# Performance work log

Measured on AMD Instinct MI355X. Metric: run time of the kernel, lower is better.

The kernel has to match this reference:

```python
import jax, jax.numpy as jnp
import numpy as np

TWO_PI = 2.0 * np.pi
SIGMA = 25.0  # marginal_prob_std sigma


def marginal_prob_std(t):
    # std(t) = sqrt((sigma^{2t} - 1) / (2 ln sigma)) for VE-SDE
    return jnp.sqrt((SIGMA ** (2.0 * t) - 1.0) / (2.0 * np.log(SIGMA)))


def edge_conv(x, src, dst, W1, b1, W2, b2, num_nodes):
    # PyG EdgeConv: msg = mlp(cat([x_i, x_j - x_i])), x_i = x[dst], x_j = x[src];
    # scatter-max over dst. First linear split so concat is never materialized:
    # cat([x_i, x_j - x_i]) @ W1 = x_i @ (Wa - Wb) + x_j @ Wb
    d = x.shape[-1]
    Wa, Wb = W1[:d], W1[d:]
    h_center = x @ (Wa - Wb)        # [N, H]
    h_nbr = x @ Wb                  # [N, H]
    e = jax.nn.relu(h_center[dst] + h_nbr[src] + b1)  # [E, H]
    e = e @ W2 + b2                 # [E, out]
    return jax.ops.segment_max(e, dst, num_segments=num_nodes)


def setup_inputs() -> dict:
    N, E, B, H, EM = 50000, 500000, 1024, 128, 64
    CLS, SD, GD, WD = 10, 4, 2, 2
    key = jax.random.key(0)
    ks = jax.random.split(key, 32)

    def lin(k, fi, fo):
        return jax.random.normal(k, (fi, fo), jnp.float32) / np.sqrt(fi)

    inp = {
        "t": jax.random.uniform(ks[0], (N, 1), jnp.float32, 1e-3, 1.0),
        "obj_x": jax.random.normal(ks[1], (N, SD), jnp.float32),
        "obj_geo": jax.random.normal(ks[2], (N, GD), jnp.float32),
        "wall": jax.random.normal(ks[3], (B, WD), jnp.float32),
        "category": jax.random.randint(ks[4], (N,), 0, CLS),
        "batch_idx": jnp.sort(jax.random.randint(ks[5], (N,), 0, B)),
        "src": jax.random.randint(ks[6], (E,), 0, N),
        "dst": jnp.tile(jnp.arange(N), E // N),  # every node receives edges
        "embed_W": jax.random.normal(ks[7], (CLS, EM), jnp.float32),
        "gfp_W": jax.random.normal(ks[8], (EM // 2,), jnp.float32) * 30.0,
        "sW": lin(ks[9], EM, EM), "sb": jnp.zeros((EM,), jnp.float32),
        "w1": lin(ks[10], WD, EM), "wb1": jnp.zeros((EM,), jnp.float32),
        "w2": lin(ks[11], EM, EM), "wb2": jnp.zeros((EM,), jnp.float32),
        "i1": lin(ks[12], SD + GD, H), "ib1": jnp.zeros((H,), jnp.float32),
        "i2": lin(ks[13], H, H), "ib2": jnp.zeros((H,), jnp.float32),
        "m1W1": lin(ks[14], 2 * (H + 3 * EM), H), "m1b1": jnp.zeros((H,), jnp.float32),
        "m1W2": lin(ks[15], H, H), "m1b2": jnp.zeros((H,), jnp.float32),
        "m2W1": lin(ks[16], 2 * (H + 3 * EM), H), "m2b1": jnp.zeros((H,), jnp.float32),
        "m2W2": lin(ks[17], H, SD), "m2b2": jnp.zeros((SD,), jnp.float32),
    }
    return inp


def reference(t, obj_x, obj_geo, wall, category, batch_idx, src, dst,
              embed_W, gfp_W, sW, sb, w1, wb1, w2, wb2,
              i1, ib1, i2, ib2, m1W1, m1b1, m1W2, m1b2,
              m2W1, m2b1, m2W2, m2b2):
    N = obj_x.shape[0]
    # conditioning features
    class_feat = jax.nn.relu(embed_W[category])                       # [N, EM]
    tv = t[:, 0]                                                      # [N]
    x_proj = tv[:, None] * gfp_W[None, :] * TWO_PI                    # [N, EM/2]
    gfp = jnp.concatenate([jnp.sin(x_proj), jnp.cos(x_proj)], axis=-1)
    sigma_feat = jax.nn.relu(gfp @ sW + sb)                           # [N, EM]
    wall_h = jax.nn.relu(jax.nn.relu(wall @ w1 + wb1) @ w2 + wb2)     # [B, EM]
    wall_feat = wall_h[batch_idx]                                     # [N, EM]
    cond = jnp.concatenate([class_feat, sigma_feat, wall_feat], axis=-1)

    # init encoder
    xin = jnp.concatenate([obj_x, obj_geo], axis=-1)                  # [N, 6]
    init = jax.nn.relu(jax.nn.relu(xin @ i1 + ib1) @ i2 + ib2)        # [N, H]

    # main backbone: two EdgeConvs with conditioning concat
    x = jnp.concatenate([init, cond], axis=-1)                        # [N, H+3EM]
    x = jax.nn.relu(edge_conv(x, src, dst, m1W1, m1b1, m1W2, m1b2, N))
    x = jnp.concatenate([x, cond], axis=-1)                           # [N, H+3EM]
    x = edge_conv(x, src, dst, m2W1, m2b1, m2W2, m2b2, N)             # [N, 4]

    return x / (marginal_prob_std(t) + 1e-7)
```

## Files before the change

kernel.cpp:

```cpp
#include <hip/hip_runtime.h>
#include <math.h>

#define NTHREADS 256
#define TWO_PI_F 6.28318530717958647692f
#define LOG_SIGMA 3.2188758248682006f

typedef unsigned short u16;
typedef unsigned int u32;
typedef short bf16x8 __attribute__((ext_vector_type(8)));
typedef float f32x4 __attribute__((ext_vector_type(4)));

#define MFMA(a, b, c) __builtin_amdgcn_mfma_f32_16x16x32_bf16((a), (b), (c), 0, 0, 0)

__device__ __forceinline__ u16 f2b(float f) {
  u32 u = __float_as_uint(f);
  u32 r = (u + 0x7fffu + ((u >> 16) & 1u)) >> 16;
  return (u16)r;
}
__device__ __forceinline__ float blo(u32 u) { return __uint_as_float(u << 16); }
__device__ __forceinline__ float bhi(u32 u) { return __uint_as_float(u & 0xffff0000u); }
__device__ __forceinline__ u32 pk(float lo, float hi) { return (u32)f2b(lo) | ((u32)f2b(hi) << 16); }

__global__ __launch_bounds__(256) void prep_kernel(
    const float* __restrict__ m1W2, const float* __restrict__ m1W1,
    const float* __restrict__ m2W1, const float* __restrict__ sW,
    const float* __restrict__ i1, const float* __restrict__ i2,
    u16* __restrict__ m1W2t, u16* __restrict__ Wc1t, u16* __restrict__ Wc2t,
    u16* __restrict__ sWt, u16* __restrict__ i1t, u16* __restrict__ i2t) {
  int idx = blockIdx.x * 256 + threadIdx.x;
  if (idx < 16384) {
    int n = idx >> 7, k = idx & 127;
    m1W2t[idx] = f2b(m1W2[k * 128 + n]);
  } else if (idx < 98304) {
    int j = idx - 16384;
    int n = j / 320, k = j - n * 320;
    float v = (n < 128) ? (m1W1[k * 128 + n] - m1W1[(320 + k) * 128 + n])
                        : m1W1[(320 + k) * 128 + (n - 128)];
    Wc1t[j] = f2b(v);
  } else if (idx < 180224) {
    int j = idx - 98304;
    int n = j / 320, k = j - n * 320;
    float v = (n < 128) ? (m2W1[k * 128 + n] - m2W1[(320 + k) * 128 + n])
                        : m2W1[(320 + k) * 128 + (n - 128)];
    Wc2t[j] = f2b(v);
  } else if (idx < 184320) {
    int j = idx - 180224;
    int n = j >> 6, k = j & 63;
    sWt[j] = f2b(sW[k * 64 + n]);
  } else if (idx < 188416) {
    int j = idx - 184320;
    int n = j >> 5, k = j & 31;
    i1t[j] = (k < 6) ? f2b(i1[k * 128 + n]) : (u16)0;
  } else if (idx < 204800) {
    int j = idx - 188416;
    int n = j >> 7, k = j & 127;
    i2t[j] = f2b(i2[k * 128 + n]);
  }
}

__global__ void wall_kernel(const float* __restrict__ wall,
                            const float* __restrict__ w1, const float* __restrict__ wb1,
                            const float* __restrict__ w2, const float* __restrict__ wb2,
                            float* __restrict__ wall_h) {
  __shared__ float h1[64];
  int b = blockIdx.x;
  int f = threadIdx.x;
  float v = wall[b * 2 + 0] * w1[f] + wall[b * 2 + 1] * w1[64 + f] + wb1[f];
  h1[f] = fmaxf(v, 0.f);
  __syncthreads();
  float acc = wb2[f];
  for (int k = 0; k < 64; ++k) acc = fmaf(h1[k], w2[k * 64 + f], acc);
  wall_h[b * 64 + f] = fmaxf(acc, 0.f);
}

__global__ __launch_bounds__(256) void node_kernel(
    const float* __restrict__ t, const float* __restrict__ obj_x,
    const float* __restrict__ obj_geo,
    const int* __restrict__ category, const int* __restrict__ batch_idx,
    const float* __restrict__ embed_W, const float* __restrict__ gfp_W,
    const u16* __restrict__ sWt, const float* __restrict__ sb,
    const u16* __restrict__ i1t, const float* __restrict__ ib1,
    const u16* __restrict__ i2t, const float* __restrict__ ib2,
    const u16* __restrict__ Wc1t, const float* __restrict__ m1b1,
    const float* __restrict__ wall_h,
    float* __restrict__ hc1, u16* __restrict__ hn1,
    u16* __restrict__ cond_bf, int N) {
  __shared__ u16 xb[64 * 328];
  __shared__ u16 ab[64 * 136];
  __shared__ float t_s[64];
  __shared__ int cat_s[64];
  __shared__ int bid_s[64];

  const int tid = threadIdx.x;
  const int base = blockIdx.x * 64;
  const int wave = tid >> 6, lane = tid & 63;
  const int ln16 = lane & 15, q8 = lane >> 4;

  bf16x8 bs0 = *(const bf16x8*)(sWt + (size_t)((wave * 16 + ln16) * 64) + q8 * 8);
  bf16x8 bs1 = *(const bf16x8*)(sWt + (size_t)((wave * 16 + ln16) * 64) + 32 + q8 * 8);
  bf16x8 bh[2];
#pragma unroll
  for (int nt = 0; nt < 2; ++nt)
    bh[nt] = *(const bf16x8*)(i1t + (size_t)((wave * 32 + nt * 16 + ln16) * 32) + q8 * 8);

  if (tid < 64) {
    int node = min(base + tid, N - 1);
    t_s[tid] = t[node];
    cat_s[tid] = category[node];
    bid_s[tid] = batch_idx[node];
  }
  __syncthreads();

  for (int idx = tid; idx < 64 * 32; idx += NTHREADS) {
    int row = idx >> 5, k = idx & 31;
    float xp = t_s[row] * gfp_W[k] * TWO_PI_F;
    float s, c;
    sincosf(xp, &s, &c);
    ab[row * 136 + k] = f2b(s);
    ab[row * 136 + 32 + k] = f2b(c);
  }
  for (int idx = tid; idx < 64 * 64; idx += NTHREADS) {
    int row = idx >> 6, f = idx & 63;
    xb[row * 328 + 128 + f] = f2b(fmaxf(embed_W[cat_s[row] * 64 + f], 0.f));
    xb[row * 328 + 256 + f] = f2b(wall_h[bid_s[row] * 64 + f]);
  }
  __syncthreads();

  f32x4 cs[4];
#pragma unroll
  for (int mt = 0; mt < 4; ++mt) cs[mt] = (f32x4)0.f;
#pragma unroll
  for (int mt = 0; mt < 4; ++mt) {
    bf16x8 a0 = *(const bf16x8*)&ab[(mt * 16 + ln16) * 136 + q8 * 8];
    cs[mt] = MFMA(a0, bs0, cs[mt]);
  }
#pragma unroll
  for (int mt = 0; mt < 4; ++mt) {
    bf16x8 a1 = *(const bf16x8*)&ab[(mt * 16 + ln16) * 136 + 32 + q8 * 8];
    cs[mt] = MFMA(a1, bs1, cs[mt]);
  }
  __syncthreads();

  {
    int col = wave * 16 + ln16;
    float bias = sb[col];
#pragma unroll
    for (int mt = 0; mt < 4; ++mt)
#pragma unroll
      for (int r = 0; r < 4; ++r)
        xb[(mt * 16 + q8 * 4 + r) * 328 + 192 + col] = f2b(fmaxf(cs[mt][r] + bias, 0.f));
  }
  for (int idx = tid; idx < 64 * 32; idx += NTHREADS) {
    int row = idx >> 5, k = idx & 31;
    int node = min(base + row, N - 1);
    float v = (k < 4) ? obj_x[node * 4 + k] : ((k < 6) ? obj_geo[node * 2 + (k - 4)] : 0.f);
    ab[row * 136 + k] = f2b(v);
  }
  __syncthreads();

  for (int idx = tid; idx < 64 * 24; idx += NTHREADS) {
    int row = idx / 24, q = idx - row * 24;
    int node = base + row;
    if (node < N)
      *(uint4*)&cond_bf[(size_t)node * 192 + q * 8] = *(uint4*)&xb[row * 328 + 128 + q * 8];
  }

  f32x4 ch[2][4];
#pragma unroll
  for (int nt = 0; nt < 2; ++nt)
#pragma unroll
    for (int mt = 0; mt < 4; ++mt) ch[nt][mt] = (f32x4)0.f;
#pragma unroll
  for (int mt = 0; mt < 4; ++mt) {
    bf16x8 a = *(const bf16x8*)&ab[(mt * 16 + ln16) * 136 + q8 * 8];
#pragma unroll
    for (int nt = 0; nt < 2; ++nt) ch[nt][mt] = MFMA(a, bh[nt], ch[nt][mt]);
  }
  bf16x8 bcur2[2], bnext2[2];
#pragma unroll
  for (int nt = 0; nt < 2; ++nt)
    bcur2[nt] = *(const bf16x8*)(i2t + (size_t)((wave * 32 + nt * 16 + ln16) * 128) + q8 * 8);
  __syncthreads();
#pragma unroll
  for (int nt = 0; nt < 2; ++nt) {
    int col = wave * 32 + nt * 16 + ln16;
    float bias = ib1[col];
#pragma unroll
    for (int mt = 0; mt < 4; ++mt)
#pragma unroll
      for (int r = 0; r < 4; ++r)
        ab[(mt * 16 + q8 * 4 + r) * 136 + col] = f2b(fmaxf(ch[nt][mt][r] + bias, 0.f));
  }
  __syncthreads();

  f32x4 ci[2][4];
#pragma unroll
  for (int nt = 0; nt < 2; ++nt)
#pragma unroll
    for (int mt = 0; mt < 4; ++mt) ci[nt][mt] = (f32x4)0.f;
  for (int kt = 0; kt < 4; ++kt) {
    if (kt < 3) {
#pragma unroll
      for (int nt = 0; nt < 2; ++nt)
        bnext2[nt] = *(const bf16x8*)(i2t + (size_t)((wave * 32 + nt * 16 + ln16) * 128) +
                                      (kt + 1) * 32 + q8 * 8);
    }
#pragma unroll
    for (int mt = 0; mt < 4; ++mt) {
      bf16x8 a = *(const bf16x8*)&ab[(mt * 16 + ln16) * 136 + kt * 32 + q8 * 8];
#pragma unroll
      for (int nt = 0; nt < 2; ++nt) ci[nt][mt] = MFMA(a, bcur2[nt], ci[nt][mt]);
    }
#pragma unroll
    for (int nt = 0; nt < 2; ++nt) bcur2[nt] = bnext2[nt];
  }
#pragma unroll
  for (int nt = 0; nt < 2; ++nt) {
    int col = wave * 32 + nt * 16 + ln16;
    float bias = ib2[col];
#pragma unroll
    for (int mt = 0; mt < 4; ++mt)
#pragma unroll
      for (int r = 0; r < 4; ++r)
        xb[(mt * 16 + q8 * 4 + r) * 328 + col] = f2b(fmaxf(ci[nt][mt][r] + bias, 0.f));
  }
  __syncthreads();

  f32x4 c2[4][4];
#pragma unroll
  for (int nt = 0; nt < 4; ++nt)
#pragma unroll
    for (int mt = 0; mt < 4; ++mt) c2[nt][mt] = (f32x4)0.f;
  bf16x8 bcur[4], bnext[4];
#pragma unroll
  for (int nt = 0; nt < 4; ++nt)
    bcur[nt] = *(const bf16x8*)(Wc1t + (size_t)((wave * 64 + nt * 16 + ln16) * 320) + q8 * 8);
  for (int kt = 0; kt < 10; ++kt) {
    if (kt < 9) {
#pragma unroll
      for (int nt = 0; nt < 4; ++nt)
        bnext[nt] = *(const bf16x8*)(Wc1t + (size_t)((wave * 64 + nt * 16 + ln16) * 320) +
                                     (kt + 1) * 32 + q8 * 8);
    }
#pragma unroll
    for (int mt = 0; mt < 4; ++mt) {
      bf16x8 a = *(const bf16x8*)&xb[(mt * 16 + ln16) * 328 + kt * 32 + q8 * 8];
#pragma unroll
      for (int nt = 0; nt < 4; ++nt) c2[nt][mt] = MFMA(a, bcur[nt], c2[nt][mt]);
    }
#pragma unroll
    for (int nt = 0; nt < 4; ++nt) bcur[nt] = bnext[nt];
  }
#pragma unroll
  for (int nt = 0; nt < 4; ++nt) {
    int col = wave * 64 + nt * 16 + ln16;
#pragma unroll
    for (int mt = 0; mt < 4; ++mt)
#pragma unroll
      for (int r = 0; r < 4; ++r) {
        int node = base + mt * 16 + q8 * 4 + r;
        if (node < N) {
          if (col < 128)
            hc1[(size_t)node * 128 + col] = c2[nt][mt][r] + m1b1[col];
          else
            hn1[(size_t)node * 128 + (col - 128)] = f2b(c2[nt][mt][r]);
        }
      }
  }
}

__global__ __launch_bounds__(256) void edge1_kernel(
    const float* __restrict__ hc1, const u16* __restrict__ hn1,
    const u16* __restrict__ cond_bf, const int* __restrict__ src,
    const u16* __restrict__ m1W2t, const float* __restrict__ m1b2,
    const u16* __restrict__ Wc2t, const float* __restrict__ m2b1,
    float* __restrict__ hc2, u16* __restrict__ hn2, int N) {
  __shared__ u16 a_lds[32 * 136];
  __shared__ u16 x2_lds[32 * 328];
  __shared__ int sid[320];

  const int tid = threadIdx.x;
  const int base = blockIdx.x * 32;
  const int wave = tid >> 6, lane = tid & 63;
  const int ln16 = lane & 15, q8 = lane >> 4;

  for (int idx = tid; idx < 320; idx += NTHREADS) {
    int e = idx >> 5, n = idx & 31;
    int node = min(base + n, N - 1);
    sid[idx] = src[node + e * N];
  }
  for (int idx = tid; idx < 768; idx += NTHREADS) {
    int n = idx / 24, q = idx - n * 24;
    int node = min(base + n, N - 1);
    *(uint4*)&x2_lds[n * 328 + 128 + q * 8] = *(const uint4*)&cond_bf[(size_t)node * 192 + q * 8];
  }
  const int ln = tid >> 3, kq = tid & 7;
  const int lnode = min(base + ln, N - 1);
  float hcr[16];
#pragma unroll
  for (int q = 0; q < 4; ++q) {
    float4 v = *(const float4*)&hc1[(size_t)lnode * 128 + kq * 16 + q * 4];
    hcr[q * 4 + 0] = v.x; hcr[q * 4 + 1] = v.y; hcr[q * 4 + 2] = v.z; hcr[q * 4 + 3] = v.w;
  }
  bf16x8 bfrag[2][4];
#pragma unroll
  for (int nt = 0; nt < 2; ++nt)
#pragma unroll
    for (int kt = 0; kt < 4; ++kt)
      bfrag[nt][kt] = *(const bf16x8*)(m1W2t + (size_t)((2 * wave + nt) * 16 + ln16) * 128 +
                                       kt * 32 + q8 * 8);

  f32x4 ymax[2][2];
#pragma unroll
  for (int mt = 0; mt < 2; ++mt)
#pragma unroll
    for (int nt = 0; nt < 2; ++nt)
#pragma unroll
      for (int r = 0; r < 4; ++r) ymax[mt][nt][r] = -3.0e38f;

  __syncthreads();

  int s = sid[ln];
  uint4 g0 = *(const uint4*)&hn1[(size_t)s * 128 + kq * 16];
  uint4 g1 = *(const uint4*)&hn1[(size_t)s * 128 + kq * 16 + 8];

  for (int e = 0; e < 10; ++e) {
    float a[16];
    a[0] = blo(g0.x); a[1] = bhi(g0.x); a[2] = blo(g0.y); a[3] = bhi(g0.y);
    a[4] = blo(g0.z); a[5] = bhi(g0.z); a[6] = blo(g0.w); a[7] = bhi(g0.w);
    a[8] = blo(g1.x); a[9] = bhi(g1.x); a[10] = blo(g1.y); a[11] = bhi(g1.y);
    a[12] = blo(g1.z); a[13] = bhi(g1.z); a[14] = blo(g1.w); a[15] = bhi(g1.w);
#pragma unroll
    for (int i = 0; i < 16; ++i) a[i] = fmaxf(hcr[i] + a[i], 0.f);
    uint4 o0, o1;
    o0.x = pk(a[0], a[1]); o0.y = pk(a[2], a[3]); o0.z = pk(a[4], a[5]); o0.w = pk(a[6], a[7]);
    o1.x = pk(a[8], a[9]); o1.y = pk(a[10], a[11]); o1.z = pk(a[12], a[13]); o1.w = pk(a[14], a[15]);
    *(uint4*)&a_lds[ln * 136 + kq * 16] = o0;
    *(uint4*)&a_lds[ln * 136 + kq * 16 + 8] = o1;
    if (e < 9) {
      s = sid[(e + 1) * 32 + ln];
      g0 = *(const uint4*)&hn1[(size_t)s * 128 + kq * 16];
      g1 = *(const uint4*)&hn1[(size_t)s * 128 + kq * 16 + 8];
    }
    __syncthreads();
    f32x4 c[2][2];
#pragma unroll
    for (int mt = 0; mt < 2; ++mt)
#pragma unroll
      for (int nt = 0; nt < 2; ++nt) c[mt][nt] = (f32x4)0.f;
#pragma unroll
    for (int kt = 0; kt < 4; ++kt) {
      bf16x8 a0 = *(const bf16x8*)&a_lds[ln16 * 136 + kt * 32 + q8 * 8];
      bf16x8 a1 = *(const bf16x8*)&a_lds[(16 + ln16) * 136 + kt * 32 + q8 * 8];
#pragma unroll
      for (int nt = 0; nt < 2; ++nt) {
        c[0][nt] = MFMA(a0, bfrag[nt][kt], c[0][nt]);
        c[1][nt] = MFMA(a1, bfrag[nt][kt], c[1][nt]);
      }
    }
#pragma unroll
    for (int mt = 0; mt < 2; ++mt)
#pragma unroll
      for (int nt = 0; nt < 2; ++nt)
#pragma unroll
        for (int r = 0; r < 4; ++r) ymax[mt][nt][r] = fmaxf(ymax[mt][nt][r], c[mt][nt][r]);
    __syncthreads();
  }

#pragma unroll
  for (int mt = 0; mt < 2; ++mt)
#pragma unroll
    for (int nt = 0; nt < 2; ++nt) {
      int col = (2 * wave + nt) * 16 + ln16;
      float bias = m1b2[col];
#pragma unroll
      for (int r = 0; r < 4; ++r) {
        int row = mt * 16 + q8 * 4 + r;
        x2_lds[row * 328 + col] = f2b(fmaxf(ymax[mt][nt][r] + bias, 0.f));
      }
    }
  __syncthreads();

  f32x4 c2[2][4];
#pragma unroll
  for (int mt = 0; mt < 2; ++mt)
#pragma unroll
    for (int nt = 0; nt < 4; ++nt) c2[mt][nt] = (f32x4)0.f;
  bf16x8 bcur[4], bnext[4];
#pragma unroll
  for (int nt = 0; nt < 4; ++nt)
    bcur[nt] = *(const bf16x8*)(Wc2t + (size_t)((wave * 4 + nt) * 16 + ln16) * 320 + q8 * 8);
  for (int kt = 0; kt < 10; ++kt) {
    if (kt < 9) {
#pragma unroll
      for (int nt = 0; nt < 4; ++nt)
        bnext[nt] = *(const bf16x8*)(Wc2t + (size_t)((wave * 4 + nt) * 16 + ln16) * 320 +
                                     (kt + 1) * 32 + q8 * 8);
    }
    bf16x8 a0 = *(const bf16x8*)&x2_lds[ln16 * 328 + kt * 32 + q8 * 8];
    bf16x8 a1 = *(const bf16x8*)&x2_lds[(16 + ln16) * 328 + kt * 32 + q8 * 8];
#pragma unroll
    for (int nt = 0; nt < 4; ++nt) {
      c2[0][nt] = MFMA(a0, bcur[nt], c2[0][nt]);
      c2[1][nt] = MFMA(a1, bcur[nt], c2[1][nt]);
    }
#pragma unroll
    for (int nt = 0; nt < 4; ++nt) bcur[nt] = bnext[nt];
  }
#pragma unroll
  for (int mt = 0; mt < 2; ++mt)
#pragma unroll
    for (int nt = 0; nt < 4; ++nt) {
      int col = (wave * 4 + nt) * 16 + ln16;
#pragma unroll
      for (int r = 0; r < 4; ++r) {
        int row = mt * 16 + q8 * 4 + r;
        int node = base + row;
        if (node < N) {
          if (wave < 2)
            hc2[(size_t)node * 128 + col] = c2[mt][nt][r] + m2b1[col];
          else
            hn2[(size_t)node * 128 + (col - 128)] = f2b(c2[mt][nt][r]);
        }
      }
    }
}

__global__ __launch_bounds__(256) void edge2_kernel(
    const float* __restrict__ hc2, const u16* __restrict__ hn2,
    const int* __restrict__ src, const float* __restrict__ t,
    const float* __restrict__ m2W2, const float* __restrict__ m2b2,
    float* __restrict__ out, int N) {
  const int tid = threadIdx.x;
  const int base = blockIdx.x * 32;
  const int ln = tid >> 3, kq = tid & 7;
  const int node = min(base + ln, N - 1);

  float hcr[16];
#pragma unroll
  for (int q = 0; q < 4; ++q) {
    float4 v = *(const float4*)&hc2[(size_t)node * 128 + kq * 16 + q * 4];
    hcr[q * 4 + 0] = v.x; hcr[q * 4 + 1] = v.y; hcr[q * 4 + 2] = v.z; hcr[q * 4 + 3] = v.w;
  }
  float w[16][4];
#pragma unroll
  for (int i = 0; i < 16; ++i) {
    float4 v = *(const float4*)&m2W2[(kq * 16 + i) * 4];
    w[i][0] = v.x; w[i][1] = v.y; w[i][2] = v.z; w[i][3] = v.w;
  }
  float ymax[4] = {-3.0e38f, -3.0e38f, -3.0e38f, -3.0e38f};

  int s = src[node];
  uint4 g0 = *(const uint4*)&hn2[(size_t)s * 128 + kq * 16];
  uint4 g1 = *(const uint4*)&hn2[(size_t)s * 128 + kq * 16 + 8];
  for (int e = 0; e < 10; ++e) {
    float a[16];
    a[0] = blo(g0.x); a[1] = bhi(g0.x); a[2] = blo(g0.y); a[3] = bhi(g0.y);
    a[4] = blo(g0.z); a[5] = bhi(g0.z); a[6] = blo(g0.w); a[7] = bhi(g0.w);
    a[8] = blo(g1.x); a[9] = bhi(g1.x); a[10] = blo(g1.y); a[11] = bhi(g1.y);
    a[12] = blo(g1.z); a[13] = bhi(g1.z); a[14] = blo(g1.w); a[15] = bhi(g1.w);
    if (e < 9) {
      s = src[node + (e + 1) * N];
      g0 = *(const uint4*)&hn2[(size_t)s * 128 + kq * 16];
      g1 = *(const uint4*)&hn2[(size_t)s * 128 + kq * 16 + 8];
    }
    float acc[4] = {0.f, 0.f, 0.f, 0.f};
#pragma unroll
    for (int i = 0; i < 16; ++i) {
      float av = fmaxf(hcr[i] + a[i], 0.f);
#pragma unroll
      for (int j = 0; j < 4; ++j) acc[j] = fmaf(av, w[i][j], acc[j]);
    }
#pragma unroll
    for (int mask = 1; mask <= 4; mask <<= 1)
#pragma unroll
      for (int j = 0; j < 4; ++j) acc[j] += __shfl_xor(acc[j], mask);
#pragma unroll
    for (int j = 0; j < 4; ++j) ymax[j] = fmaxf(ymax[j], acc[j]);
  }
  if (kq < 4 && base + ln < N) {
    float tv = t[node];
    float mps = sqrtf((expf(2.f * tv * LOG_SIGMA) - 1.f) * (1.f / (2.f * LOG_SIGMA)));
    out[(size_t)node * 4 + kq] = (ymax[kq] + m2b2[kq]) / (mps + 1e-7f);
  }
}

extern "C" void kernel_launch(void* const* d_in, const int* in_sizes, int n_in,
                              void* d_out, int out_size, void* d_ws, size_t ws_size,
                              hipStream_t stream) {
  const float* t = (const float*)d_in[0];
  const float* obj_x = (const float*)d_in[1];
  const float* obj_geo = (const float*)d_in[2];
  const float* wall = (const float*)d_in[3];
  const int* category = (const int*)d_in[4];
  const int* batch_idx = (const int*)d_in[5];
  const int* src = (const int*)d_in[6];
  const float* embed_W = (const float*)d_in[8];
  const float* gfp_W = (const float*)d_in[9];
  const float* sW = (const float*)d_in[10];
  const float* sb = (const float*)d_in[11];
  const float* w1 = (const float*)d_in[12];
  const float* wb1 = (const float*)d_in[13];
  const float* w2 = (const float*)d_in[14];
  const float* wb2 = (const float*)d_in[15];
  const float* i1 = (const float*)d_in[16];
  const float* ib1 = (const float*)d_in[17];
  const float* i2 = (const float*)d_in[18];
  const float* ib2 = (const float*)d_in[19];
  const float* m1W1 = (const float*)d_in[20];
  const float* m1b1 = (const float*)d_in[21];
  const float* m1W2 = (const float*)d_in[22];
  const float* m1b2 = (const float*)d_in[23];
  const float* m2W1 = (const float*)d_in[24];
  const float* m2b1 = (const float*)d_in[25];
  const float* m2W2 = (const float*)d_in[26];
  const float* m2b2 = (const float*)d_in[27];
  float* out = (float*)d_out;

  const int N = in_sizes[0];
  const int B = in_sizes[3] / 2;

  char* w = (char*)d_ws;
  float* wall_h = (float*)w; w += (size_t)B * 64 * 4;
  u16* cond_bf = (u16*)w;   w += (size_t)N * 192 * 2;
  float* hc1 = (float*)w;   w += (size_t)N * 128 * 4;
  u16* hn1 = (u16*)w;       w += (size_t)N * 128 * 2;
  float* hc2 = (float*)w;   w += (size_t)N * 128 * 4;
  u16* hn2 = (u16*)w;       w += (size_t)N * 128 * 2;
  u16* m1W2t = (u16*)w;     w += (size_t)128 * 128 * 2;
  u16* Wc1t = (u16*)w;      w += (size_t)256 * 320 * 2;
  u16* Wc2t = (u16*)w;      w += (size_t)256 * 320 * 2;
  u16* sWt = (u16*)w;       w += (size_t)64 * 64 * 2;
  u16* i1t = (u16*)w;       w += (size_t)128 * 32 * 2;
  u16* i2t = (u16*)w;       w += (size_t)128 * 128 * 2;

  prep_kernel<<<dim3(800), dim3(256), 0, stream>>>(m1W2, m1W1, m2W1, sW, i1, i2,
                                                   m1W2t, Wc1t, Wc2t, sWt, i1t, i2t);
  wall_kernel<<<dim3(B), dim3(64), 0, stream>>>(wall, w1, wb1, w2, wb2, wall_h);
  node_kernel<<<dim3((N + 63) / 64), dim3(NTHREADS), 0, stream>>>(
      t, obj_x, obj_geo, category, batch_idx, embed_W, gfp_W, sWt, sb,
      i1t, ib1, i2t, ib2, Wc1t, m1b1, wall_h, hc1, hn1, cond_bf, N);
  edge1_kernel<<<dim3((N + 31) / 32), dim3(NTHREADS), 0, stream>>>(
      hc1, hn1, cond_bf, src, m1W2t, m1b2, Wc2t, m2b1, hc2, hn2, N);
  edge2_kernel<<<dim3((N + 31) / 32), dim3(NTHREADS), 0, stream>>>(
      hc2, hn2, src, t, m2W2, m2b2, out, N);
}
```

Before: 294.0 us.

## Switch pipeline to fp16, restructure edge1 to register-resident MFMA operands

All intermediates and weights move from bf16/fp32 to fp16, and the MFMA intrinsic becomes the f16 variant. hc1/hc2 are now stored as fp16 instead of fp32, which halves their memory traffic. edge1 no longer stages the relu'd edge messages through LDS with two barriers per edge. Each wave instead builds its MFMA A-operand directly from gathered registers, using packed half2 add and relu over a 16-row by 64-column tile, and gets a launch-bounds occupancy hint. edge2 uses packed fp16 dot2 with pre-transposed fp16 weights; the trade-off is a narrower fp16 range and precision for activations.

Result: slower. 301.9 us (+2.7%).

```diff
diff --git a/kernel.cpp b/kernel.cpp
--- a/kernel.cpp
+++ b/kernel.cpp
@@ -7,54 +7,64 @@
 
 typedef unsigned short u16;
 typedef unsigned int u32;
-typedef short bf16x8 __attribute__((ext_vector_type(8)));
+typedef _Float16 f16x2 __attribute__((ext_vector_type(2)));
+typedef _Float16 f16x8 __attribute__((ext_vector_type(8)));
 typedef float f32x4 __attribute__((ext_vector_type(4)));
 
-#define MFMA(a, b, c) __builtin_amdgcn_mfma_f32_16x16x32_bf16((a), (b), (c), 0, 0, 0)
-
-__device__ __forceinline__ u16 f2b(float f) {
-  u32 u = __float_as_uint(f);
-  u32 r = (u + 0x7fffu + ((u >> 16) & 1u)) >> 16;
-  return (u16)r;
-}
-__device__ __forceinline__ float blo(u32 u) { return __uint_as_float(u << 16); }
-__device__ __forceinline__ float bhi(u32 u) { return __uint_as_float(u & 0xffff0000u); }
-__device__ __forceinline__ u32 pk(float lo, float hi) { return (u32)f2b(lo) | ((u32)f2b(hi) << 16); }
+#define MFMA16(a, b, c) __builtin_amdgcn_mfma_f32_16x16x32_f16((a), (b), (c), 0, 0, 0)
+
+__device__ __forceinline__ u16 f2h(float f) {
+  _Float16 h = (_Float16)f;
+  union { _Float16 h; u16 u; } cv;
+  cv.h = h;
+  return cv.u;
+}
+__device__ __forceinline__ f16x2 relu2(f16x2 x) {
+  f16x2 z;
+  z[0] = (_Float16)0.f; z[1] = (_Float16)0.f;
+  return __builtin_elementwise_max(x, z);
+}
 
 __global__ __launch_bounds__(256) void prep_kernel(
     const float* __restrict__ m1W2, const float* __restrict__ m1W1,
     const float* __restrict__ m2W1, const float* __restrict__ sW,
     const float* __restrict__ i1, const float* __restrict__ i2,
+    const float* __restrict__ m2W2,
     u16* __restrict__ m1W2t, u16* __restrict__ Wc1t, u16* __restrict__ Wc2t,
-    u16* __restrict__ sWt, u16* __restrict__ i1t, u16* __restrict__ i2t) {
+    u16* __restrict__ sWt, u16* __restrict__ i1t, u16* __restrict__ i2t,
+    u16* __restrict__ m2W2t) {
   int idx = blockIdx.x * 256 + threadIdx.x;
   if (idx < 16384) {
     int n = idx >> 7, k = idx & 127;
-    m1W2t[idx] = f2b(m1W2[k * 128 + n]);
+    m1W2t[idx] = f2h(m1W2[k * 128 + n]);
   } else if (idx < 98304) {
     int j = idx - 16384;
     int n = j / 320, k = j - n * 320;
     float v = (n < 128) ? (m1W1[k * 128 + n] - m1W1[(320 + k) * 128 + n])
                         : m1W1[(320 + k) * 128 + (n - 128)];
-    Wc1t[j] = f2b(v);
+    Wc1t[j] = f2h(v);
   } else if (idx < 180224) {
     int j = idx - 98304;
     int n = j / 320, k = j - n * 320;
     float v = (n < 128) ? (m2W1[k * 128 + n] - m2W1[(320 + k) * 128 + n])
                         : m2W1[(320 + k) * 128 + (n - 128)];
-    Wc2t[j] = f2b(v);
+    Wc2t[j] = f2h(v);
   } else if (idx < 184320) {
     int j = idx - 180224;
     int n = j >> 6, k = j & 63;
-    sWt[j] = f2b(sW[k * 64 + n]);
+    sWt[j] = f2h(sW[k * 64 + n]);
   } else if (idx < 188416) {
     int j = idx - 184320;
     int n = j >> 5, k = j & 31;
-    i1t[j] = (k < 6) ? f2b(i1[k * 128 + n]) : (u16)0;
+    i1t[j] = (k < 6) ? f2h(i1[k * 128 + n]) : (u16)0;
   } else if (idx < 204800) {
     int j = idx - 188416;
     int n = j >> 7, k = j & 127;
-    i2t[j] = f2b(i2[k * 128 + n]);
+    i2t[j] = f2h(i2[k * 128 + n]);
+  } else if (idx < 205312) {
+    int j = idx - 204800;
+    int n = j >> 7, k = j & 127;
+    m2W2t[j] = f2h(m2W2[k * 4 + n]);
   }
 }
 
@@ -83,8 +93,8 @@
     const u16* __restrict__ i2t, const float* __restrict__ ib2,
     const u16* __restrict__ Wc1t, const float* __restrict__ m1b1,
     const float* __restrict__ wall_h,
-    float* __restrict__ hc1, u16* __restrict__ hn1,
-    u16* __restrict__ cond_bf, int N) {
+    u16* __restrict__ hc1f, u16* __restrict__ hn1f,
+    u16* __restrict__ cond_h, int N) {
   __shared__ u16 xb[64 * 328];
   __shared__ u16 ab[64 * 136];
   __shared__ float t_s[64];
@@ -96,12 +106,12 @@
   const int wave = tid >> 6, lane = tid & 63;
   const int ln16 = lane & 15, q8 = lane >> 4;
 
-  bf16x8 bs0 = *(const bf16x8*)(sWt + (size_t)((wave * 16 + ln16) * 64) + q8 * 8);
-  bf16x8 bs1 = *(const bf16x8*)(sWt + (size_t)((wave * 16 + ln16) * 64) + 32 + q8 * 8);
-  bf16x8 bh[2];
+  f16x8 bs0 = *(const f16x8*)(sWt + (size_t)((wave * 16 + ln16) * 64) + q8 * 8);
+  f16x8 bs1 = *(const f16x8*)(sWt + (size_t)((wave * 16 + ln16) * 64) + 32 + q8 * 8);
+  f16x8 bh[2];
 #pragma unroll
   for (int nt = 0; nt < 2; ++nt)
-    bh[nt] = *(const bf16x8*)(i1t + (size_t)((wave * 32 + nt * 16 + ln16) * 32) + q8 * 8);
+    bh[nt] = *(const f16x8*)(i1t + (size_t)((wave * 32 + nt * 16 + ln16) * 32) + q8 * 8);
 
   if (tid < 64) {
     int node = min(base + tid, N - 1);
@@ -116,13 +126,13 @@
     float xp = t_s[row] * gfp_W[k] * TWO_PI_F;
     float s, c;
     sincosf(xp, &s, &c);
-    ab[row * 136 + k] = f2b(s);
-    ab[row * 136 + 32 + k] = f2b(c);
+    ab[row * 136 + k] = f2h(s);
+    ab[row * 136 + 32 + k] = f2h(c);
   }
   for (int idx = tid; idx < 64 * 64; idx += NTHREADS) {
     int row = idx >> 6, f = idx & 63;
-    xb[row * 328 + 128 + f] = f2b(fmaxf(embed_W[cat_s[row] * 64 + f], 0.f));
-    xb[row * 328 + 256 + f] = f2b(wall_h[bid_s[row] * 64 + f]);
+    xb[row * 328 + 128 + f] = f2h(fmaxf(embed_W[cat_s[row] * 64 + f], 0.f));
+    xb[row * 328 + 256 + f] = f2h(wall_h[bid_s[row] * 64 + f]);
   }
   __syncthreads();
 
@@ -131,13 +141,13 @@
   for (int mt = 0; mt < 4; ++mt) cs[mt] = (f32x4)0.f;
 #pragma unroll
   for (int mt = 0; mt < 4; ++mt) {
-    bf16x8 a0 = *(const bf16x8*)&ab[(mt * 16 + ln16) * 136 + q8 * 8];
-    cs[mt] = MFMA(a0, bs0, cs[mt]);
+    f16x8 a0 = *(const f16x8*)&ab[(mt * 16 + ln16) * 136 + q8 * 8];
+    cs[mt] = MFMA16(a0, bs0, cs[mt]);
   }
 #pragma unroll
   for (int mt = 0; mt < 4; ++mt) {
-    bf16x8 a1 = *(const bf16x8*)&ab[(mt * 16 + ln16) * 136 + 32 + q8 * 8];
-    cs[mt] = MFMA(a1, bs1, cs[mt]);
+    f16x8 a1 = *(const f16x8*)&ab[(mt * 16 + ln16) * 136 + 32 + q8 * 8];
+    cs[mt] = MFMA16(a1, bs1, cs[mt]);
   }
   __syncthreads();
 
@@ -148,13 +158,13 @@
     for (int mt = 0; mt < 4; ++mt)
 #pragma unroll
       for (int r = 0; r < 4; ++r)
-        xb[(mt * 16 + q8 * 4 + r) * 328 + 192 + col] = f2b(fmaxf(cs[mt][r] + bias, 0.f));
+        xb[(mt * 16 + q8 * 4 + r) * 328 + 192 + col] = f2h(fmaxf(cs[mt][r] + bias, 0.f));
   }
   for (int idx = tid; idx < 64 * 32; idx += NTHREADS) {
     int row = idx >> 5, k = idx & 31;
     int node = min(base + row, N - 1);
     float v = (k < 4) ? obj_x[node * 4 + k] : ((k < 6) ? obj_geo[node * 2 + (k - 4)] : 0.f);
-    ab[row * 136 + k] = f2b(v);
+    ab[row * 136 + k] = f2h(v);
   }
   __syncthreads();
 
@@ -162,7 +172,7 @@
     int row = idx / 24, q = idx - row * 24;
     int node = base + row;
     if (node < N)
-      *(uint4*)&cond_bf[(size_t)node * 192 + q * 8] = *(uint4*)&xb[row * 328 + 128 + q * 8];
+      *(uint4*)&cond_h[(size_t)node * 192 + q * 8] = *(uint4*)&xb[row * 328 + 128 + q * 8];
   }
 
   f32x4 ch[2][4];
@@ -172,14 +182,14 @@
     for (int mt = 0; mt < 4; ++mt) ch[nt][mt] = (f32x4)0.f;
 #pragma unroll
   for (int mt = 0; mt < 4; ++mt) {
-    bf16x8 a = *(const bf16x8*)&ab[(mt * 16 + ln16) * 136 + q8 * 8];
-#pragma unroll
-    for (int nt = 0; nt < 2; ++nt) ch[nt][mt] = MFMA(a, bh[nt], ch[nt][mt]);
-  }
-  bf16x8 bcur2[2], bnext2[2];
+    f16x8 a = *(const f16x8*)&ab[(mt * 16 + ln16) * 136 + q8 * 8];
+#pragma unroll
+    for (int nt = 0; nt < 2; ++nt) ch[nt][mt] = MFMA16(a, bh[nt], ch[nt][mt]);
+  }
+  f16x8 bcur2[2], bnext2[2];
 #pragma unroll
   for (int nt = 0; nt < 2; ++nt)
-    bcur2[nt] = *(const bf16x8*)(i2t + (size_t)((wave * 32 + nt * 16 + ln16) * 128) + q8 * 8);
+    bcur2[nt] = *(const f16x8*)(i2t + (size_t)((wave * 32 + nt * 16 + ln16) * 128) + q8 * 8);
   __syncthreads();
 #pragma unroll
   for (int nt = 0; nt < 2; ++nt) {
@@ -189,7 +199,7 @@
     for (int mt = 0; mt < 4; ++mt)
 #pragma unroll
       for (int r = 0; r < 4; ++r)
-        ab[(mt * 16 + q8 * 4 + r) * 136 + col] = f2b(fmaxf(ch[nt][mt][r] + bias, 0.f));
+        ab[(mt * 16 + q8 * 4 + r) * 136 + col] = f2h(fmaxf(ch[nt][mt][r] + bias, 0.f));
   }
   __syncthreads();
 
@@ -202,14 +212,14 @@
     if (kt < 3) {
 #pragma unroll
       for (int nt = 0; nt < 2; ++nt)
-        bnext2[nt] = *(const bf16x8*)(i2t + (size_t)((wave * 32 + nt * 16 + ln16) * 128) +
-                                      (kt + 1) * 32 + q8 * 8);
+        bnext2[nt] = *(const f16x8*)(i2t + (size_t)((wave * 32 + nt * 16 + ln16) * 128) +
+                                     (kt + 1) * 32 + q8 * 8);
     }
 #pragma unroll
     for (int mt = 0; mt < 4; ++mt) {
-      bf16x8 a = *(const bf16x8*)&ab[(mt * 16 + ln16) * 136 + kt * 32 + q8 * 8];
-#pragma unroll
-      for (int nt = 0; nt < 2; ++nt) ci[nt][mt] = MFMA(a, bcur2[nt], ci[nt][mt]);
+      f16x8 a = *(const f16x8*)&ab[(mt * 16 + ln16) * 136 + kt * 32 + q8 * 8];
+#pragma unroll
+      for (int nt = 0; nt < 2; ++nt) ci[nt][mt] = MFMA16(a, bcur2[nt], ci[nt][mt]);
     }
 #pragma unroll
     for (int nt = 0; nt < 2; ++nt) bcur2[nt] = bnext2[nt];
@@ -222,7 +232,7 @@
     for (int mt = 0; mt < 4; ++mt)
 #pragma unroll
       for (int r = 0; r < 4; ++r)
-        xb[(mt * 16 + q8 * 4 + r) * 328 + col] = f2b(fmaxf(ci[nt][mt][r] + bias, 0.f));
+        xb[(mt * 16 + q8 * 4 + r) * 328 + col] = f2h(fmaxf(ci[nt][mt][r] + bias, 0.f));
   }
   __syncthreads();
 
@@ -231,22 +241,22 @@
   for (int nt = 0; nt < 4; ++nt)
 #pragma unroll
     for (int mt = 0; mt < 4; ++mt) c2[nt][mt] = (f32x4)0.f;
-  bf16x8 bcur[4], bnext[4];
+  f16x8 bcur[4], bnext[4];
 #pragma unroll
   for (int nt = 0; nt < 4; ++nt)
-    bcur[nt] = *(const bf16x8*)(Wc1t + (size_t)((wave * 64 + nt * 16 + ln16) * 320) + q8 * 8);
+    bcur[nt] = *(const f16x8*)(Wc1t + (size_t)((wave * 64 + nt * 16 + ln16) * 320) + q8 * 8);
   for (int kt = 0; kt < 10; ++kt) {
     if (kt < 9) {
 #pragma unroll
       for (int nt = 0; nt < 4; ++nt)
-        bnext[nt] = *(const bf16x8*)(Wc1t + (size_t)((wave * 64 + nt * 16 + ln16) * 320) +
-                                     (kt + 1) * 32 + q8 * 8);
+        bnext[nt] = *(const f16x8*)(Wc1t + (size_t)((wave * 64 + nt * 16 + ln16) * 320) +
+                                    (kt + 1) * 32 + q8 * 8);
     }
 #pragma unroll
     for (int mt = 0; mt < 4; ++mt) {
-      bf16x8 a = *(const bf16x8*)&xb[(mt * 16 + ln16) * 328 + kt * 32 + q8 * 8];
-#pragma unroll
-      for (int nt = 0; nt < 4; ++nt) c2[nt][mt] = MFMA(a, bcur[nt], c2[nt][mt]);
+      f16x8 a = *(const f16x8*)&xb[(mt * 16 + ln16) * 328 + kt * 32 + q8 * 8];
+#pragma unroll
+      for (int nt = 0; nt < 4; ++nt) c2[nt][mt] = MFMA16(a, bcur[nt], c2[nt][mt]);
     }
 #pragma unroll
     for (int nt = 0; nt < 4; ++nt) bcur[nt] = bnext[nt];
@@ -261,21 +271,20 @@
         int node = base + mt * 16 + q8 * 4 + r;
         if (node < N) {
           if (col < 128)
-            hc1[(size_t)node * 128 + col] = c2[nt][mt][r] + m1b1[col];
+            hc1f[(size_t)node * 128 + col] = f2h(c2[nt][mt][r] + m1b1[col]);
           else
-            hn1[(size_t)node * 128 + (col - 128)] = f2b(c2[nt][mt][r]);
+            hn1f[(size_t)node * 128 + (col - 128)] = f2h(c2[nt][mt][r]);
         }
       }
   }
 }
 
-__global__ __launch_bounds__(256) void edge1_kernel(
-    const float* __restrict__ hc1, const u16* __restrict__ hn1,
-    const u16* __restrict__ cond_bf, const int* __restrict__ src,
+__global__ __launch_bounds__(256, 3) void edge1_kernel(
+    const u16* __restrict__ hc1f, const u16* __restrict__ hn1f,
+    const u16* __restrict__ cond_h, const int* __restrict__ src,
     const u16* __restrict__ m1W2t, const float* __restrict__ m1b2,
     const u16* __restrict__ Wc2t, const float* __restrict__ m2b1,
-    float* __restrict__ hc2, u16* __restrict__ hn2, int N) {
-  __shared__ u16 a_lds[32 * 136];
+    u16* __restrict__ hc2f, u16* __restrict__ hn2f, int N) {
   __shared__ u16 x2_lds[32 * 328];
   __shared__ int sid[320];
 
@@ -283,193 +292,185 @@
   const int base = blockIdx.x * 32;
   const int wave = tid >> 6, lane = tid & 63;
   const int ln16 = lane & 15, q8 = lane >> 4;
+  const int rowoff = (wave >> 1) * 16;
+  const int colh = (wave & 1) * 64;
+  const int myrow = rowoff + ln16;
+  const int mynode = min(base + myrow, N - 1);
 
   for (int idx = tid; idx < 320; idx += NTHREADS) {
     int e = idx >> 5, n = idx & 31;
-    int node = min(base + n, N - 1);
-    sid[idx] = src[node + e * N];
+    sid[idx] = src[min(base + n, N - 1) + e * N];
   }
   for (int idx = tid; idx < 768; idx += NTHREADS) {
     int n = idx / 24, q = idx - n * 24;
-    int node = min(base + n, N - 1);
-    *(uint4*)&x2_lds[n * 328 + 128 + q * 8] = *(const uint4*)&cond_bf[(size_t)node * 192 + q * 8];
-  }
-  const int ln = tid >> 3, kq = tid & 7;
-  const int lnode = min(base + ln, N - 1);
-  float hcr[16];
-#pragma unroll
-  for (int q = 0; q < 4; ++q) {
-    float4 v = *(const float4*)&hc1[(size_t)lnode * 128 + kq * 16 + q * 4];
-    hcr[q * 4 + 0] = v.x; hcr[q * 4 + 1] = v.y; hcr[q * 4 + 2] = v.z; hcr[q * 4 + 3] = v.w;
-  }
-  bf16x8 bfrag[2][4];
-#pragma unroll
-  for (int nt = 0; nt < 2; ++nt)
+    int nd = min(base + n, N - 1);
+    *(uint4*)&x2_lds[n * 328 + 128 + q * 8] = *(const uint4*)&cond_h[(size_t)nd * 192 + q * 8];
+  }
+
+  uint4 hc4[4];
+#pragma unroll
+  for (int kt = 0; kt < 4; ++kt)
+    hc4[kt] = *(const uint4*)&hc1f[(size_t)mynode * 128 + kt * 32 + q8 * 8];
+
+  f16x8 bfr[4][4];
+#pragma unroll
+  for (int nt = 0; nt < 4; ++nt)
 #pragma unroll
     for (int kt = 0; kt < 4; ++kt)
-      bfrag[nt][kt] = *(const bf16x8*)(m1W2t + (size_t)((2 * wave + nt) * 16 + ln16) * 128 +
-                                       kt * 32 + q8 * 8);
-
-  f32x4 ymax[2][2];
+      bfr[nt][kt] = *(const f16x8*)(m1W2t + (size_t)(colh + nt * 16 + ln16) * 128 +
+                                    kt * 32 + q8 * 8);
+  __syncthreads();
+
+  f32x4 ymax[4];
+#pragma unroll
+  for (int nt = 0; nt < 4; ++nt)
+#pragma unroll
+    for (int r = 0; r < 4; ++r) ymax[nt][r] = -3.0e38f;
+
+  uint4 g[4], gn[4];
+  {
+    int s = sid[myrow];
+#pragma unroll
+    for (int kt = 0; kt < 4; ++kt)
+      g[kt] = *(const uint4*)&hn1f[(size_t)s * 128 + kt * 32 + q8 * 8];
+  }
+  for (int e = 0; e < 10; ++e) {
+    if (e < 9) {
+      int s = sid[(e + 1) * 32 + myrow];
+#pragma unroll
+      for (int kt = 0; kt < 4; ++kt)
+        gn[kt] = *(const uint4*)&hn1f[(size_t)s * 128 + kt * 32 + q8 * 8];
+    }
+#pragma unroll
+    for (int kt = 0; kt < 4; ++kt) {
+      f16x2* gp = (f16x2*)&g[kt];
+      const f16x2* hp = (const f16x2*)&hc4[kt];
+#pragma unroll
+      for (int p = 0; p < 4; ++p) gp[p] = relu2(gp[p] + hp[p]);
+    }
+    f32x4 c[4];
+#pragma unroll
+    for (int nt = 0; nt < 4; ++nt) c[nt] = (f32x4)0.f;
+#pragma unroll
+    for (int kt = 0; kt < 4; ++kt) {
+      f16x8 a = *(const f16x8*)&g[kt];
+#pragma unroll
+      for (int nt = 0; nt < 4; ++nt) c[nt] = MFMA16(a, bfr[nt][kt], c[nt]);
+    }
+#pragma unroll
+    for (int nt = 0; nt < 4; ++nt)
+#pragma unroll
+      for (int r = 0; r < 4; ++r) ymax[nt][r] = fmaxf(ymax[nt][r], c[nt][r]);
+#pragma unroll
+    for (int kt = 0; kt < 4; ++kt) g[kt] = gn[kt];
+  }
+
+#pragma unroll
+  for (int nt = 0; nt < 4; ++nt) {
+    int col = colh + nt * 16 + ln16;
+    float bias = m1b2[col];
+#pragma unroll
+    for (int r = 0; r < 4; ++r) {
+      int row = rowoff + q8 * 4 + r;
+      x2_lds[row * 328 + col] = f2h(fmaxf(ymax[nt][r] + bias, 0.f));
+    }
+  }
+  __syncthreads();
+
+  f32x4 c2[2][4];
 #pragma unroll
   for (int mt = 0; mt < 2; ++mt)
 #pragma unroll
-    for (int nt = 0; nt < 2; ++nt)
-#pragma unroll
-      for (int r = 0; r < 4; ++r) ymax[mt][nt][r] = -3.0e38f;
-
-  __syncthreads();
-
-  int s = sid[ln];
-  uint4 g0 = *(const uint4*)&hn1[(size_t)s * 128 + kq * 16];
-  uint4 g1 = *(const uint4*)&hn1[(size_t)s * 128 + kq * 16 + 8];
-
-  for (int e = 0; e < 10; ++e) {
-    float a[16];
-    a[0] = blo(g0.x); a[1] = bhi(g0.x); a[2] = blo(g0.y); a[3] = bhi(g0.y);
-    a[4] = blo(g0.z); a[5] = bhi(g0.z); a[6] = blo(g0.w); a[7] = bhi(g0.w);
-    a[8] = blo(g1.x); a[9] = bhi(g1.x); a[10] = blo(g1.y); a[11] = bhi(g1.y);
-    a[12] = blo(g1.z); a[13] = bhi(g1.z); a[14] = blo(g1.w); a[15] = bhi(g1.w);
-#pragma unroll
-    for (int i = 0; i < 16; ++i) a[i] = fmaxf(hcr[i] + a[i], 0.f);
-    uint4 o0, o1;
-    o0.x = pk(a[0], a[1]); o0.y = pk(a[2], a[3]); o0.z = pk(a[4], a[5]); o0.w = pk(a[6], a[7]);
-    o1.x = pk(a[8], a[9]); o1.y = pk(a[10], a[11]); o1.z = pk(a[12], a[13]); o1.w = pk(a[14], a[15]);
-    *(uint4*)&a_lds[ln * 136 + kq * 16] = o0;
-    *(uint4*)&a_lds[ln * 136 + kq * 16 + 8] = o1;
-    if (e < 9) {
-      s = sid[(e + 1) * 32 + ln];
-      g0 = *(const uint4*)&hn1[(size_t)s * 128 + kq * 16];
-      g1 = *(const uint4*)&hn1[(size_t)s * 128 + kq * 16 + 8];
-    }
-    __syncthreads();
-    f32x4 c[2][2];
-#pragma unroll
-    for (int mt = 0; mt < 2; ++mt)
-#pragma unroll
-      for (int nt = 0; nt < 2; ++nt) c[mt][nt] = (f32x4)0.f;
-#pragma unroll
-    for (int kt = 0; kt < 4; ++kt) {
-      bf16x8 a0 = *(const bf16x8*)&a_lds[ln16 * 136 + kt * 32 + q8 * 8];
-      bf16x8 a1 = *(const bf16x8*)&a_lds[(16 + ln16) * 136 + kt * 32 + q8 * 8];
-#pragma unroll
-      for (int nt = 0; nt < 2; ++nt) {
-        c[0][nt] = MFMA(a0, bfrag[nt][kt], c[0][nt]);
-        c[1][nt] = MFMA(a1, bfrag[nt][kt], c[1][nt]);
-      }
-    }
-#pragma unroll
-    for (int mt = 0; mt < 2; ++mt)
-#pragma unroll
-      for (int nt = 0; nt < 2; ++nt)
-#pragma unroll
-        for (int r = 0; r < 4; ++r) ymax[mt][nt][r] = fmaxf(ymax[mt][nt][r], c[mt][nt][r]);
-    __syncthreads();
-  }
-
-#pragma unroll
-  for (int mt = 0; mt < 2; ++mt)
-#pragma unroll
-    for (int nt = 0; nt < 2; ++nt) {
-      int col = (2 * wave + nt) * 16 + ln16;
-      float bias = m1b2[col];
-#pragma unroll
-      for (int r = 0; r < 4; ++r) {
-        int row = mt * 16 + q8 * 4 + r;
-        x2_lds[row * 328 + col] = f2b(fmaxf(ymax[mt][nt][r] + bias, 0.f));
-      }
-    }
-  __syncthreads();
-
-  f32x4 c2[2][4];
-#pragma unroll
-  for (int mt = 0; mt < 2; ++mt)
-#pragma unroll
     for (int nt = 0; nt < 4; ++nt) c2[mt][nt] = (f32x4)0.f;
-  bf16x8 bcur[4], bnext[4];
+  f16x8 bcur[4], bnext[4];
 #pragma unroll
   for (int nt = 0; nt < 4; ++nt)
-    bcur[nt] = *(const bf16x8*)(Wc2t + (size_t)((wave * 4 + nt) * 16 + ln16) * 320 + q8 * 8);
+    bcur[nt] = *(const f16x8*)(Wc2t + (size_t)(wave * 64 + nt * 16 + ln16) * 320 + q8 * 8);
   for (int kt = 0; kt < 10; ++kt) {
     if (kt < 9) {
 #pragma unroll
       for (int nt = 0; nt < 4; ++nt)
-        bnext[nt] = *(const bf16x8*)(Wc2t + (size_t)((wave * 4 + nt) * 16 + ln16) * 320 +
-                                     (kt + 1) * 32 + q8 * 8);
-    }
-    bf16x8 a0 = *(const bf16x8*)&x2_lds[ln16 * 328 + kt * 32 + q8 * 8];
-    bf16x8 a1 = *(const bf16x8*)&x2_lds[(16 + ln16) * 328 + kt * 32 + q8 * 8];
+        bnext[nt] = *(const f16x8*)(Wc2t + (size_t)(wave * 64 + nt * 16 + ln16) * 320 +
+                                    (kt + 1) * 32 + q8 * 8);
+    }
+    f16x8 a0 = *(const f16x8*)&x2_lds[ln16 * 328 + kt * 32 + q8 * 8];
+    f16x8 a1 = *(const f16x8*)&x2_lds[(16 + ln16) * 328 + kt * 32 + q8 * 8];
 #pragma unroll
     for (int nt = 0; nt < 4; ++nt) {
-      c2[0][nt] = MFMA(a0, bcur[nt], c2[0][nt]);
-      c2[1][nt] = MFMA(a1, bcur[nt], c2[1][nt]);
+      c2[0][nt] = MFMA16(a0, bcur[nt], c2[0][nt]);
+      c2[1][nt] = MFMA16(a1, bcur[nt], c2[1][nt]);
     }
 #pragma unroll
     for (int nt = 0; nt < 4; ++nt) bcur[nt] = bnext[nt];
   }
 #pragma unroll
-  for (int mt = 0; mt < 2; ++mt)
-#pragma unroll
-    for (int nt = 0; nt < 4; ++nt) {
-      int col = (wave * 4 + nt) * 16 + ln16;
+  for (int nt = 0; nt < 4; ++nt) {
+    int col = wave * 64 + nt * 16 + ln16;
+#pragma unroll
+    for (int mt = 0; mt < 2; ++mt)
 #pragma unroll
       for (int r = 0; r < 4; ++r) {
-        int row = mt * 16 + q8 * 4 + r;
-        int node = base + row;
+        int node = base + mt * 16 + q8 * 4 + r;
         if (node < N) {
-          if (wave < 2)
-            hc2[(size_t)node * 128 + col] = c2[mt][nt][r] + m2b1[col];
+          if (col < 128)
+            hc2f[(size_t)node * 128 + col] = f2h(c2[mt][nt][r] + m2b1[col]);
           else
-            hn2[(size_t)node * 128 + (col - 128)] = f2b(c2[mt][nt][r]);
+            hn2f[(size_t)node * 128 + (col - 128)] = f2h(c2[mt][nt][r]);
         }
       }
-    }
+  }
 }
 
 __global__ __launch_bounds__(256) void edge2_kernel(
-    const float* __restrict__ hc2, const u16* __restrict__ hn2,
+    const u16* __restrict__ hc2f, const u16* __restrict__ hn2f,
     const int* __restrict__ src, const float* __restrict__ t,
-    const float* __restrict__ m2W2, const float* __restrict__ m2b2,
+    const u16* __restrict__ m2W2t, const float* __restrict__ m2b2,
     float* __restrict__ out, int N) {
   const int tid = threadIdx.x;
   const int base = blockIdx.x * 32;
   const int ln = tid >> 3, kq = tid & 7;
   const int node = min(base + ln, N - 1);
 
-  float hcr[16];
-#pragma unroll
-  for (int q = 0; q < 4; ++q) {
-    float4 v = *(const float4*)&hc2[(size_t)node * 128 + kq * 16 + q * 4];
-    hcr[q * 4 + 0] = v.x; hcr[q * 4 + 1] = v.y; hcr[q * 4 + 2] = v.z; hcr[q * 4 + 3] = v.w;
-  }
-  float w[16][4];
-#pragma unroll
-  for (int i = 0; i < 16; ++i) {
-    float4 v = *(const float4*)&m2W2[(kq * 16 + i) * 4];
-    w[i][0] = v.x; w[i][1] = v.y; w[i][2] = v.z; w[i][3] = v.w;
+  uint4 hc0 = *(const uint4*)&hc2f[(size_t)node * 128 + kq * 16];
+  uint4 hc1_ = *(const uint4*)&hc2f[(size_t)node * 128 + kq * 16 + 8];
+  uint4 w4[4][2];
+#pragma unroll
+  for (int j = 0; j < 4; ++j) {
+    w4[j][0] = *(const uint4*)&m2W2t[j * 128 + kq * 16];
+    w4[j][1] = *(const uint4*)&m2W2t[j * 128 + kq * 16 + 8];
   }
   float ymax[4] = {-3.0e38f, -3.0e38f, -3.0e38f, -3.0e38f};
 
   int s = src[node];
-  uint4 g0 = *(const uint4*)&hn2[(size_t)s * 128 + kq * 16];
-  uint4 g1 = *(const uint4*)&hn2[(size_t)s * 128 + kq * 16 + 8];
+  uint4 g0 = *(const uint4*)&hn2f[(size_t)s * 128 + kq * 16];
+  uint4 g1 = *(const uint4*)&hn2f[(size_t)s * 128 + kq * 16 + 8];
   for (int e = 0; e < 10; ++e) {
-    float a[16];
-    a[0] = blo(g0.x); a[1] = bhi(g0.x); a[2] = blo(g0.y); a[3] = bhi(g0.y);
-    a[4] = blo(g0.z); a[5] = bhi(g0.z); a[6] = blo(g0.w); a[7] = bhi(g0.w);
-    a[8] = blo(g1.x); a[9] = bhi(g1.x); a[10] = blo(g1.y); a[11] = bhi(g1.y);
-    a[12] = blo(g1.z); a[13] = bhi(g1.z); a[14] = blo(g1.w); a[15] = bhi(g1.w);
+    f16x2 a2[8];
+    {
+      const f16x2* gp0 = (const f16x2*)&g0;
+      const f16x2* gp1 = (const f16x2*)&g1;
+      const f16x2* hp0 = (const f16x2*)&hc0;
+      const f16x2* hp1 = (const f16x2*)&hc1_;
+#pragma unroll
+      for (int p = 0; p < 4; ++p) a2[p] = relu2(gp0[p] + hp0[p]);
+#pragma unroll
+      for (int p = 0; p < 4; ++p) a2[4 + p] = relu2(gp1[p] + hp1[p]);
+    }
     if (e < 9) {
       s = src[node + (e + 1) * N];
-      g0 = *(const uint4*)&hn2[(size_t)s * 128 + kq * 16];
-      g1 = *(const uint4*)&hn2[(size_t)s * 128 + kq * 16 + 8];
+      g0 = *(const uint4*)&hn2f[(size_t)s * 128 + kq * 16];
+      g1 = *(const uint4*)&hn2f[(size_t)s * 128 + kq * 16 + 8];
     }
     float acc[4] = {0.f, 0.f, 0.f, 0.f};
 #pragma unroll
-    for (int i = 0; i < 16; ++i) {
-      float av = fmaxf(hcr[i] + a[i], 0.f);
-#pragma unroll
-      for (int j = 0; j < 4; ++j) acc[j] = fmaf(av, w[i][j], acc[j]);
+    for (int j = 0; j < 4; ++j) {
+      const f16x2* wp0 = (const f16x2*)&w4[j][0];
+      const f16x2* wp1 = (const f16x2*)&w4[j][1];
+#pragma unroll
+      for (int p = 0; p < 4; ++p) {
+        acc[j] = __builtin_amdgcn_fdot2(a2[p], wp0[p], acc[j], false);
+        acc[j] = __builtin_amdgcn_fdot2(a2[4 + p], wp1[p], acc[j], false);
+      }
     }
 #pragma unroll
     for (int mask = 1; mask <= 4; mask <<= 1)
@@ -522,26 +523,27 @@
 
   char* w = (char*)d_ws;
   float* wall_h = (float*)w; w += (size_t)B * 64 * 4;
-  u16* cond_bf = (u16*)w;   w += (size_t)N * 192 * 2;
-  float* hc1 = (float*)w;   w += (size_t)N * 128 * 4;
-  u16* hn1 = (u16*)w;       w += (size_t)N * 128 * 2;
-  float* hc2 = (float*)w;   w += (size_t)N * 128 * 4;
-  u16* hn2 = (u16*)w;       w += (size_t)N * 128 * 2;
+  u16* cond_h = (u16*)w;    w += (size_t)N * 192 * 2;
+  u16* hc1f = (u16*)w;      w += (size_t)N * 128 * 2;
+  u16* hn1f = (u16*)w;      w += (size_t)N * 128 * 2;
+  u16* hc2f = (u16*)w;      w += (size_t)N * 128 * 2;
+  u16* hn2f = (u16*)w;      w += (size_t)N * 128 * 2;
   u16* m1W2t = (u16*)w;     w += (size_t)128 * 128 * 2;
   u16* Wc1t = (u16*)w;      w += (size_t)256 * 320 * 2;
   u16* Wc2t = (u16*)w;      w += (size_t)256 * 320 * 2;
   u16* sWt = (u16*)w;       w += (size_t)64 * 64 * 2;
   u16* i1t = (u16*)w;       w += (size_t)128 * 32 * 2;
   u16* i2t = (u16*)w;       w += (size_t)128 * 128 * 2;
-
-  prep_kernel<<<dim3(800), dim3(256), 0, stream>>>(m1W2, m1W1, m2W1, sW, i1, i2,
-                                                   m1W2t, Wc1t, Wc2t, sWt, i1t, i2t);
+  u16* m2W2t = (u16*)w;     w += (size_t)4 * 128 * 2;
+
+  prep_kernel<<<dim3(802), dim3(256), 0, stream>>>(m1W2, m1W1, m2W1, sW, i1, i2, m2W2,
+                                                   m1W2t, Wc1t, Wc2t, sWt, i1t, i2t, m2W2t);
   wall_kernel<<<dim3(B), dim3(64), 0, stream>>>(wall, w1, wb1, w2, wb2, wall_h);
   node_kernel<<<dim3((N + 63) / 64), dim3(NTHREADS), 0, stream>>>(
       t, obj_x, obj_geo, category, batch_idx, embed_W, gfp_W, sWt, sb,
-      i1t, ib1, i2t, ib2, Wc1t, m1b1, wall_h, hc1, hn1, cond_bf, N);
+      i1t, ib1, i2t, ib2, Wc1t, m1b1, wall_h, hc1f, hn1f, cond_h, N);
   edge1_kernel<<<dim3((N + 31) / 32), dim3(NTHREADS), 0, stream>>>(
-      hc1, hn1, cond_bf, src, m1W2t, m1b2, Wc2t, m2b1, hc2, hn2, N);
+      hc1f, hn1f, cond_h, src, m1W2t, m1b2, Wc2t, m2b1, hc2f, hn2f, N);
   edge2_kernel<<<dim3((N + 31) / 32), dim3(NTHREADS), 0, stream>>>(
-      hc2, hn2, src, t, m2W2, m2b2, out, N);
-}
+      hc2f, hn2f, src, t, m2W2t, m2b2, out, N);
+}
```
